# Kernel optimization log

Hardware: AMD Instinct MI355X
Metric: run time of the kernel (lower is better)

The kernel has to match this reference:

```python
import jax, jax.numpy as jnp
import numpy as np

N_HEAD = 16
WINDOW = 128
CAUSAL = False


def setup_inputs() -> dict:
    key = jax.random.key(0)
    ks = jax.random.split(key, 5)
    B, T, D = 1, 4096, 1024
    x = jax.random.normal(ks[0], (B, T, D), dtype=jnp.float32)
    w_in = jax.random.normal(ks[1], (3 * D, D), dtype=jnp.float32) * 0.02
    b_in = jax.random.normal(ks[2], (3 * D,), dtype=jnp.float32) * 0.02
    w_out = jax.random.normal(ks[3], (D, D), dtype=jnp.float32) * 0.02
    b_out = jax.random.normal(ks[4], (D,), dtype=jnp.float32) * 0.02
    return {"x": x, "w_in": w_in, "b_in": b_in, "w_out": w_out, "b_out": b_out}


def _window_attention(x, w_in, b_in, w_out, b_out):
    B, T, D = x.shape
    H = N_HEAD
    hd = D // H
    scale = 1.0 / jnp.sqrt(jnp.float32(hd))

    # fused in-projection, as in torch nn.MultiheadAttention (y = x @ W^T + b)
    qkv = jnp.einsum('btd,ed->bte', x, w_in) + b_in  # (B, T, 3D)
    q, k, v = jnp.split(qkv, 3, axis=-1)
    # (B, H, T, hd)
    q = q.reshape(B, T, H, hd).transpose(0, 2, 1, 3)
    k = k.reshape(B, T, H, hd).transpose(0, 2, 1, 3)
    v = v.reshape(B, T, H, hd).transpose(0, 2, 1, 3)

    scores = jnp.einsum('bhqd,bhkd->bhqk', q, k) * scale  # (B, H, T, T)

    idx = jnp.arange(T)
    diff = idx[:, None] - idx[None, :]
    if CAUSAL:
        allowed = (diff >= 0) & (diff <= WINDOW)
    else:
        allowed = jnp.abs(diff) <= WINDOW
    NEG = jnp.float32(-1e30)
    scores = jnp.where(allowed[None, None, :, :], scores, NEG)

    attn = jax.nn.softmax(scores, axis=-1)
    ctx = jnp.einsum('bhqk,bhkd->bhqd', attn, v)  # (B, H, T, hd)
    ctx = ctx.transpose(0, 2, 1, 3).reshape(B, T, D)
    out = jnp.einsum('btd,ed->bte', ctx, w_out) + b_out
    return x + out  # residual, as in the module


def reference(x, w_in, b_in, w_out, b_out):
    return _window_attention(x, w_in, b_in, w_out, b_out)
```

## Files before the change

kernel.cpp:

```cpp
#include <hip/hip_runtime.h>

#define T_SEQ 4096
#define DMODEL 1024
#define NHEAD 16
#define HDIM 64
#define WIN 128

typedef __attribute__((ext_vector_type(8))) short bf16x8;
typedef __attribute__((ext_vector_type(4))) float f32x4;
typedef __attribute__((ext_vector_type(4))) unsigned short u16x4;

__device__ __forceinline__ unsigned short f2bf(float f) {
  unsigned int u = __builtin_bit_cast(unsigned int, f);
  return (unsigned short)((u + 0x7fffu + ((u >> 16) & 1u)) >> 16);
}

__device__ __forceinline__ void gload_lds16(const unsigned short* g,
                                            unsigned short* l) {
  __builtin_amdgcn_global_load_lds(
      (const __attribute__((address_space(1))) void*)g,
      (__attribute__((address_space(3))) void*)l, 16, 0, 0);
}

__global__ void convert_all(const float* __restrict__ x,
                            const float* __restrict__ w_in,
                            const float* __restrict__ w_out,
                            unsigned short* __restrict__ x_bf,
                            unsigned short* __restrict__ w_in_bf,
                            unsigned short* __restrict__ w_out_bf) {
  int stride = gridDim.x * blockDim.x;
  int t0 = blockIdx.x * blockDim.x + threadIdx.x;
#define CVT(SRC, DST, N4)                                          \
  for (int i = t0; i < (N4); i += stride) {                        \
    float4 v = reinterpret_cast<const float4*>(SRC)[i];            \
    u16x4 o;                                                       \
    o.x = f2bf(v.x); o.y = f2bf(v.y); o.z = f2bf(v.z); o.w = f2bf(v.w); \
    reinterpret_cast<u16x4*>(DST)[i] = o;                          \
  }
  CVT(x, x_bf, T_SEQ * DMODEL / 4)
  CVT(w_in, w_in_bf, 3 * DMODEL * DMODEL / 4)
  CVT(w_out, w_out_bf, DMODEL * DMODEL / 4)
#undef CVT
}

template <int EPI, int BM, int BN>
__global__ __launch_bounds__(256) void gemm_db(
    const unsigned short* __restrict__ A,
    const unsigned short* __restrict__ B,
    const float* __restrict__ bias,
    unsigned short* __restrict__ q_buf,
    unsigned short* __restrict__ k_buf,
    unsigned short* __restrict__ vt_buf,
    const float* __restrict__ x_res,
    float* __restrict__ out) {
  const int K = DMODEL;
  constexpr int NT = DMODEL / 64;
  constexpr int SM = BM / 2, SN = BN / 2;
  constexpr int MR = SM / 16, NR = SN / 16;
  constexpr int AL = BM / 32, BL = BN / 32;
  __shared__ __align__(16) unsigned short As[2 * BM * 64];
  __shared__ __align__(16) unsigned short Bs[2 * BN * 64];

  int tid = threadIdx.x;
  int lane = tid & 63, wave = tid >> 6;
  int wr = wave >> 1, wc = wave & 1;
  int lo = lane & 15, hi = lane >> 4;
  int t0 = blockIdx.y * BM, e0 = blockIdx.x * BN;

  f32x4 acc[MR][NR];
#pragma unroll
  for (int m = 0; m < MR; ++m)
#pragma unroll
    for (int n = 0; n < NR; ++n) acc[m][n] = (f32x4){0.f, 0.f, 0.f, 0.f};

  int c8 = (tid & 7) ^ ((tid >> 3) & 7);
  int srow = tid >> 3;
  const unsigned short* AbaseG = A + (size_t)(t0 + srow) * K + c8 * 8;
  const unsigned short* BbaseG = B + (size_t)(e0 + srow) * K + c8 * 8;
  unsigned short* ldsAu = As + wave * 512;
  unsigned short* ldsBu = Bs + wave * 512;

  auto stage = [&](int tt) {
    int k0 = tt * 64;
    int ab = (tt & 1) * (BM * 64);
    int bb = (tt & 1) * (BN * 64);
#pragma unroll
    for (int l = 0; l < AL; ++l)
      gload_lds16(AbaseG + (size_t)l * 32 * K + k0, ldsAu + l * 2048 + ab);
#pragma unroll
    for (int l = 0; l < BL; ++l)
      gload_lds16(BbaseG + (size_t)l * 32 * K + k0, ldsBu + l * 2048 + bb);
  };

  stage(0);
  asm volatile("s_waitcnt vmcnt(0) lgkmcnt(0)\n\ts_barrier" ::: "memory");

  for (int t = 0; t < NT; ++t) {
    if (t + 1 < NT) stage(t + 1);
    const unsigned short* Ab = As + (t & 1) * (BM * 64);
    const unsigned short* Bb = Bs + (t & 1) * (BN * 64);
    bf16x8 af[MR][2], bfr[NR][2];
#pragma unroll
    for (int m = 0; m < MR; ++m) {
      int row = wr * SM + m * 16 + lo;
#pragma unroll
      for (int ks = 0; ks < 2; ++ks)
        af[m][ks] = *reinterpret_cast<const bf16x8*>(
            &Ab[row * 64 + (((ks << 2) + hi) ^ (row & 7)) * 8]);
    }
#pragma unroll
    for (int n = 0; n < NR; ++n) {
      int row = wc * SN + n * 16 + lo;
#pragma unroll
      for (int ks = 0; ks < 2; ++ks)
        bfr[n][ks] = *reinterpret_cast<const bf16x8*>(
            &Bb[row * 64 + (((ks << 2) + hi) ^ (row & 7)) * 8]);
    }
#pragma unroll
    for (int ks = 0; ks < 2; ++ks)
#pragma unroll
      for (int m = 0; m < MR; ++m)
#pragma unroll
        for (int n = 0; n < NR; ++n)
          acc[m][n] = __builtin_amdgcn_mfma_f32_16x16x32_bf16(af[m][ks], bfr[n][ks],
                                                              acc[m][n], 0, 0, 0);
    asm volatile("s_waitcnt vmcnt(0) lgkmcnt(0)\n\ts_barrier" ::: "memory");
  }

  int t0w = t0 + wr * SM;
  int e0w = e0 + wc * SN;
#pragma unroll
  for (int m = 0; m < MR; ++m) {
#pragma unroll
    for (int n = 0; n < NR; ++n) {
      int e = e0w + n * 16 + lo;
      float bv = bias[e];
      if (EPI == 0) {
        int part = e >> 10;
        int h = (e >> 6) & 15;
        int d = e & 63;
        if (part == 2) {
          int t = t0w + m * 16 + hi * 4;
          u16x4 pk;
          pk.x = f2bf(acc[m][n][0] + bv);
          pk.y = f2bf(acc[m][n][1] + bv);
          pk.z = f2bf(acc[m][n][2] + bv);
          pk.w = f2bf(acc[m][n][3] + bv);
          *reinterpret_cast<u16x4*>(&vt_buf[((size_t)(h * HDIM + d)) * T_SEQ + t]) = pk;
        } else {
          unsigned short* dst = (part == 0) ? q_buf : k_buf;
#pragma unroll
          for (int j = 0; j < 4; ++j) {
            int t = t0w + m * 16 + hi * 4 + j;
            dst[((size_t)h * T_SEQ + t) * HDIM + d] = f2bf(acc[m][n][j] + bv);
          }
        }
      } else {
#pragma unroll
        for (int j = 0; j < 4; ++j) {
          int t = t0w + m * 16 + hi * 4 + j;
          size_t idx = (size_t)t * DMODEL + e;
          out[idx] = acc[m][n][j] + bv + x_res[idx];
        }
      }
    }
  }
}

__global__ __launch_bounds__(256) void win_attn(
    const unsigned short* __restrict__ q_buf,
    const unsigned short* __restrict__ k_buf,
    const unsigned short* __restrict__ vt_buf,
    unsigned short* __restrict__ ctx) {
  __shared__ __align__(16) unsigned short p_lds[4][2][16 * 40];
  int tid = threadIdx.x;
  int wave = tid >> 6;
  int lane = tid & 63;
  int lo = lane & 15, hi = lane >> 4;

  int id = blockIdx.x;
  int sw = (id & 7) * (512 / 8) + (id >> 3);
  int job = sw * 4 + wave;
  int h = job >> 7;
  int q0 = (job & 127) * 32;
  const float SC = 0.18033688011112042f;

  bf16x8 aq[2][2];
#pragma unroll
  for (int u = 0; u < 2; ++u) {
    const unsigned short* qrow =
        q_buf + ((size_t)h * T_SEQ + q0 + u * 16 + lo) * HDIM + hi * 8;
    aq[u][0] = *reinterpret_cast<const bf16x8*>(qrow);
    aq[u][1] = *reinterpret_cast<const bf16x8*>(qrow + 32);
  }

  float L[2][4] = {{0.f, 0.f, 0.f, 0.f}, {0.f, 0.f, 0.f, 0.f}};
  f32x4 o[2][4];
#pragma unroll
  for (int u = 0; u < 2; ++u)
#pragma unroll
    for (int n = 0; n < 4; ++n) o[u][n] = (f32x4){0.f, 0.f, 0.f, 0.f};

  int jstart = q0 - WIN; if (jstart < 0) jstart = 0;
  int jend = q0 + 32 + WIN; if (jend > T_SEQ) jend = T_SEQ;

  bf16x8 kc[2][2];
#pragma unroll
  for (int c = 0; c < 2; ++c) {
    const unsigned short* kp =
        k_buf + ((size_t)h * T_SEQ + jstart + c * 16 + lo) * HDIM + hi * 8;
    kc[c][0] = *reinterpret_cast<const bf16x8*>(kp);
    kc[c][1] = *reinterpret_cast<const bf16x8*>(kp + 32);
  }

  for (int j0 = jstart; j0 < jend; j0 += 32) {
    int jn = (j0 + 32 < jend) ? j0 + 32 : jstart;
    bf16x8 kn[2][2];
#pragma unroll
    for (int c = 0; c < 2; ++c) {
      const unsigned short* kp =
          k_buf + ((size_t)h * T_SEQ + jn + c * 16 + lo) * HDIM + hi * 8;
      kn[c][0] = *reinterpret_cast<const bf16x8*>(kp);
      kn[c][1] = *reinterpret_cast<const bf16x8*>(kp + 32);
    }
    bf16x8 bv[4];
#pragma unroll
    for (int n = 0; n < 4; ++n)
      bv[n] = *reinterpret_cast<const bf16x8*>(
          vt_buf + ((size_t)(h * HDIM + n * 16 + lo)) * T_SEQ + j0 + hi * 8);
#pragma unroll
    for (int u = 0; u < 2; ++u) {
#pragma unroll
      for (int c = 0; c < 2; ++c) {
        f32x4 z = (f32x4){0.f, 0.f, 0.f, 0.f};
        z = __builtin_amdgcn_mfma_f32_16x16x32_bf16(aq[u][0], kc[c][0], z, 0, 0, 0);
        z = __builtin_amdgcn_mfma_f32_16x16x32_bf16(aq[u][1], kc[c][1], z, 0, 0, 0);
        int kj = j0 + c * 16 + lo;
#pragma unroll
        for (int j = 0; j < 4; ++j) {
          int q = q0 + u * 16 + hi * 4 + j;
          bool ok = (q - kj <= WIN) && (kj - q <= WIN);
          float p = ok ? __builtin_amdgcn_exp2f(z[j] * SC) : 0.f;
          L[u][j] += p;
          p_lds[wave][u][(hi * 4 + j) * 40 + c * 16 + lo] = f2bf(p);
        }
      }
    }
    bf16x8 pa[2];
    pa[0] = *reinterpret_cast<const bf16x8*>(&p_lds[wave][0][lo * 40 + hi * 8]);
    pa[1] = *reinterpret_cast<const bf16x8*>(&p_lds[wave][1][lo * 40 + hi * 8]);
#pragma unroll
    for (int n = 0; n < 4; ++n) {
      o[0][n] = __builtin_amdgcn_mfma_f32_16x16x32_bf16(pa[0], bv[n], o[0][n], 0, 0, 0);
      o[1][n] = __builtin_amdgcn_mfma_f32_16x16x32_bf16(pa[1], bv[n], o[1][n], 0, 0, 0);
    }
#pragma unroll
    for (int c = 0; c < 2; ++c) {
      kc[c][0] = kn[c][0];
      kc[c][1] = kn[c][1];
    }
  }
#pragma unroll
  for (int u = 0; u < 2; ++u)
#pragma unroll
    for (int j = 0; j < 4; ++j) {
#pragma unroll
      for (int w = 1; w < 16; w <<= 1) L[u][j] += __shfl_xor(L[u][j], w, 64);
    }
#pragma unroll
  for (int u = 0; u < 2; ++u)
#pragma unroll
    for (int j = 0; j < 4; ++j) {
      int t = q0 + u * 16 + hi * 4 + j;
      float inv = 1.f / L[u][j];
#pragma unroll
      for (int n = 0; n < 4; ++n)
        ctx[(size_t)t * DMODEL + h * HDIM + n * 16 + lo] = f2bf(o[u][n][j] * inv);
    }
}

extern "C" void kernel_launch(void* const* d_in, const int* in_sizes, int n_in,
                              void* d_out, int out_size, void* d_ws, size_t ws_size,
                              hipStream_t stream) {
  const float* x = (const float*)d_in[0];
  const float* w_in = (const float*)d_in[1];
  const float* b_in = (const float*)d_in[2];
  const float* w_out = (const float*)d_in[3];
  const float* b_out = (const float*)d_in[4];
  float* out = (float*)d_out;

  char* ws = (char*)d_ws;
  size_t off = 0;
  auto take = [&](size_t bytes) {
    char* p = ws + off;
    off += (bytes + 255) & ~(size_t)255;
    return p;
  };
  unsigned short* x_bf = (unsigned short*)take((size_t)T_SEQ * DMODEL * 2);
  unsigned short* w_in_bf = (unsigned short*)take((size_t)3 * DMODEL * DMODEL * 2);
  unsigned short* w_out_bf = (unsigned short*)take((size_t)DMODEL * DMODEL * 2);
  unsigned short* q_buf = (unsigned short*)take((size_t)T_SEQ * DMODEL * 2);
  unsigned short* k_buf = (unsigned short*)take((size_t)T_SEQ * DMODEL * 2);
  unsigned short* vt_buf = (unsigned short*)take((size_t)T_SEQ * DMODEL * 2 + 8192);
  unsigned short* ctx = (unsigned short*)take((size_t)T_SEQ * DMODEL * 2);

  convert_all<<<2048, 256, 0, stream>>>(x, w_in, w_out, x_bf, w_in_bf, w_out_bf);

  dim3 g1(3 * DMODEL / 192, T_SEQ / 128);
  gemm_db<0, 128, 192><<<g1, 256, 0, stream>>>(x_bf, w_in_bf, b_in, q_buf, k_buf,
                                               vt_buf, nullptr, nullptr);

  win_attn<<<512, 256, 0, stream>>>(q_buf, k_buf, vt_buf, ctx);

  dim3 g2(DMODEL / 64, T_SEQ / 128);
  gemm_db<1, 128, 64><<<g2, 256, 0, stream>>>(ctx, w_out_bf, b_out, nullptr, nullptr,
                                              nullptr, x, out);
}
```

Measured before the change: 89.20 us.

## Enlarge GEMM tiles to 256 rows with 512 threads and XCD-aware block mapping

Both projection GEMMs now use 256-row tiles computed by 8 waves (512 threads), and the 2D grid becomes a 1D grid of 256 blocks. Block indices are remapped so blocks landing on the same XCD share row strips, which should improve L2 reuse of the A operand. The inner loop now loads fragments per k-substep to lower register pressure. The trade-off is fewer blocks, exactly 256 for 256 CUs, so there is no spare occupancy, plus more LDS per block. The out-projection's remap covers 16 column tiles of 64, which matches D=1024.

```diff
diff --git a/kernel.cpp b/kernel.cpp
--- a/kernel.cpp
+++ b/kernel.cpp
@@ -44,7 +44,7 @@
 }
 
 template <int EPI, int BM, int BN>
-__global__ __launch_bounds__(256) void gemm_db(
+__global__ __launch_bounds__(512) void gemm_db(
     const unsigned short* __restrict__ A,
     const unsigned short* __restrict__ B,
     const float* __restrict__ bias,
@@ -55,9 +55,9 @@
     float* __restrict__ out) {
   const int K = DMODEL;
   constexpr int NT = DMODEL / 64;
-  constexpr int SM = BM / 2, SN = BN / 2;
+  constexpr int SM = 64, SN = BN / 2;
   constexpr int MR = SM / 16, NR = SN / 16;
-  constexpr int AL = BM / 32, BL = BN / 32;
+  constexpr int AL = BM / 64, BL = BN / 64;
   __shared__ __align__(16) unsigned short As[2 * BM * 64];
   __shared__ __align__(16) unsigned short Bs[2 * BN * 64];
 
@@ -65,7 +65,12 @@
   int lane = tid & 63, wave = tid >> 6;
   int wr = wave >> 1, wc = wave & 1;
   int lo = lane & 15, hi = lane >> 4;
-  int t0 = blockIdx.y * BM, e0 = blockIdx.x * BN;
+
+  int idx = blockIdx.x;
+  int xcd = idx & 7, j = idx >> 3;
+  int bx = j & 15;
+  int by = xcd * 2 + (j >> 4);
+  int t0 = by * BM, e0 = bx * BN;
 
   f32x4 acc[MR][NR];
 #pragma unroll
@@ -86,10 +91,10 @@
     int bb = (tt & 1) * (BN * 64);
 #pragma unroll
     for (int l = 0; l < AL; ++l)
-      gload_lds16(AbaseG + (size_t)l * 32 * K + k0, ldsAu + l * 2048 + ab);
+      gload_lds16(AbaseG + (size_t)l * 64 * K + k0, ldsAu + l * 4096 + ab);
 #pragma unroll
     for (int l = 0; l < BL; ++l)
-      gload_lds16(BbaseG + (size_t)l * 32 * K + k0, ldsBu + l * 2048 + bb);
+      gload_lds16(BbaseG + (size_t)l * 64 * K + k0, ldsBu + l * 4096 + bb);
   };
 
   stage(0);
@@ -99,31 +104,28 @@
     if (t + 1 < NT) stage(t + 1);
     const unsigned short* Ab = As + (t & 1) * (BM * 64);
     const unsigned short* Bb = Bs + (t & 1) * (BN * 64);
-    bf16x8 af[MR][2], bfr[NR][2];
-#pragma unroll
-    for (int m = 0; m < MR; ++m) {
-      int row = wr * SM + m * 16 + lo;
-#pragma unroll
-      for (int ks = 0; ks < 2; ++ks)
-        af[m][ks] = *reinterpret_cast<const bf16x8*>(
+#pragma unroll
+    for (int ks = 0; ks < 2; ++ks) {
+      bf16x8 af[MR], bfr[NR];
+#pragma unroll
+      for (int m = 0; m < MR; ++m) {
+        int row = wr * SM + m * 16 + lo;
+        af[m] = *reinterpret_cast<const bf16x8*>(
             &Ab[row * 64 + (((ks << 2) + hi) ^ (row & 7)) * 8]);
-    }
-#pragma unroll
-    for (int n = 0; n < NR; ++n) {
-      int row = wc * SN + n * 16 + lo;
-#pragma unroll
-      for (int ks = 0; ks < 2; ++ks)
-        bfr[n][ks] = *reinterpret_cast<const bf16x8*>(
+      }
+#pragma unroll
+      for (int n = 0; n < NR; ++n) {
+        int row = wc * SN + n * 16 + lo;
+        bfr[n] = *reinterpret_cast<const bf16x8*>(
             &Bb[row * 64 + (((ks << 2) + hi) ^ (row & 7)) * 8]);
-    }
-#pragma unroll
-    for (int ks = 0; ks < 2; ++ks)
+      }
 #pragma unroll
       for (int m = 0; m < MR; ++m)
 #pragma unroll
         for (int n = 0; n < NR; ++n)
-          acc[m][n] = __builtin_amdgcn_mfma_f32_16x16x32_bf16(af[m][ks], bfr[n][ks],
+          acc[m][n] = __builtin_amdgcn_mfma_f32_16x16x32_bf16(af[m], bfr[n],
                                                               acc[m][n], 0, 0, 0);
+    }
     asm volatile("s_waitcnt vmcnt(0) lgkmcnt(0)\n\ts_barrier" ::: "memory");
   }
 
@@ -150,17 +152,17 @@
         } else {
           unsigned short* dst = (part == 0) ? q_buf : k_buf;
 #pragma unroll
-          for (int j = 0; j < 4; ++j) {
-            int t = t0w + m * 16 + hi * 4 + j;
-            dst[((size_t)h * T_SEQ + t) * HDIM + d] = f2bf(acc[m][n][j] + bv);
+          for (int jj = 0; jj < 4; ++jj) {
+            int t = t0w + m * 16 + hi * 4 + jj;
+            dst[((size_t)h * T_SEQ + t) * HDIM + d] = f2bf(acc[m][n][jj] + bv);
           }
         }
       } else {
 #pragma unroll
-        for (int j = 0; j < 4; ++j) {
-          int t = t0w + m * 16 + hi * 4 + j;
-          size_t idx = (size_t)t * DMODEL + e;
-          out[idx] = acc[m][n][j] + bv + x_res[idx];
+        for (int jj = 0; jj < 4; ++jj) {
+          int t = t0w + m * 16 + hi * 4 + jj;
+          size_t idxo = (size_t)t * DMODEL + e;
+          out[idxo] = acc[m][n][jj] + bv + x_res[idxo];
         }
       }
     }
@@ -237,12 +239,12 @@
         z = __builtin_amdgcn_mfma_f32_16x16x32_bf16(aq[u][1], kc[c][1], z, 0, 0, 0);
         int kj = j0 + c * 16 + lo;
 #pragma unroll
-        for (int j = 0; j < 4; ++j) {
-          int q = q0 + u * 16 + hi * 4 + j;
+        for (int jq = 0; jq < 4; ++jq) {
+          int q = q0 + u * 16 + hi * 4 + jq;
           bool ok = (q - kj <= WIN) && (kj - q <= WIN);
-          float p = ok ? __builtin_amdgcn_exp2f(z[j] * SC) : 0.f;
-          L[u][j] += p;
-          p_lds[wave][u][(hi * 4 + j) * 40 + c * 16 + lo] = f2bf(p);
+          float p = ok ? __builtin_amdgcn_exp2f(z[jq] * SC) : 0.f;
+          L[u][jq] += p;
+          p_lds[wave][u][(hi * 4 + jq) * 40 + c * 16 + lo] = f2bf(p);
         }
       }
     }
@@ -263,19 +265,19 @@
 #pragma unroll
   for (int u = 0; u < 2; ++u)
 #pragma unroll
-    for (int j = 0; j < 4; ++j) {
-#pragma unroll
-      for (int w = 1; w < 16; w <<= 1) L[u][j] += __shfl_xor(L[u][j], w, 64);
+    for (int jq = 0; jq < 4; ++jq) {
+#pragma unroll
+      for (int w = 1; w < 16; w <<= 1) L[u][jq] += __shfl_xor(L[u][jq], w, 64);
     }
 #pragma unroll
   for (int u = 0; u < 2; ++u)
 #pragma unroll
-    for (int j = 0; j < 4; ++j) {
-      int t = q0 + u * 16 + hi * 4 + j;
-      float inv = 1.f / L[u][j];
+    for (int jq = 0; jq < 4; ++jq) {
+      int t = q0 + u * 16 + hi * 4 + jq;
+      float inv = 1.f / L[u][jq];
 #pragma unroll
       for (int n = 0; n < 4; ++n)
-        ctx[(size_t)t * DMODEL + h * HDIM + n * 16 + lo] = f2bf(o[u][n][j] * inv);
+        ctx[(size_t)t * DMODEL + h * HDIM + n * 16 + lo] = f2bf(o[u][n][jq] * inv);
     }
 }
 
@@ -306,13 +308,11 @@
 
   convert_all<<<2048, 256, 0, stream>>>(x, w_in, w_out, x_bf, w_in_bf, w_out_bf);
 
-  dim3 g1(3 * DMODEL / 192, T_SEQ / 128);
-  gemm_db<0, 128, 192><<<g1, 256, 0, stream>>>(x_bf, w_in_bf, b_in, q_buf, k_buf,
-                                               vt_buf, nullptr, nullptr);
+  gemm_db<0, 256, 192><<<256, 512, 0, stream>>>(x_bf, w_in_bf, b_in, q_buf, k_buf,
+                                                vt_buf, nullptr, nullptr);
 
   win_attn<<<512, 256, 0, stream>>>(q_buf, k_buf, vt_buf, ctx);
 
-  dim3 g2(DMODEL / 64, T_SEQ / 128);
-  gemm_db<1, 128, 64><<<g2, 256, 0, stream>>>(ctx, w_out_bf, b_out, nullptr, nullptr,
-                                              nullptr, x, out);
-}
+  gemm_db<1, 256, 64><<<256, 512, 0, stream>>>(ctx, w_out_bf, b_out, nullptr, nullptr,
+                                               nullptr, x, out);
+}
```

After: 89.48 us. No clear change (+0.3%).

## Split attention key range across wave pairs and merge partial results via LDS

Applied to the files above, without the earlier changes.

Each query tile in the windowed attention kernel is now processed by two waves, each handling half of the key range, and the grid doubles to 1024 blocks. Partial outputs and row sums are exchanged through a new shared-memory buffer and combined, with each wave writing half of the rows. The change also raises wave priority around MFMA instructions and wraps the GEMM template in two named kernels. It aims to add parallelism and shorten the serial key loop per wave, at the cost of extra LDS traffic, a block barrier and larger shared memory use.

```diff
diff --git a/kernel.cpp b/kernel.cpp
--- a/kernel.cpp
+++ b/kernel.cpp
@@ -44,7 +44,7 @@
 }
 
 template <int EPI, int BM, int BN>
-__global__ __launch_bounds__(256) void gemm_db(
+__device__ __forceinline__ void gemm_body(
     const unsigned short* __restrict__ A,
     const unsigned short* __restrict__ B,
     const float* __restrict__ bias,
@@ -150,21 +150,35 @@
         } else {
           unsigned short* dst = (part == 0) ? q_buf : k_buf;
 #pragma unroll
-          for (int j = 0; j < 4; ++j) {
-            int t = t0w + m * 16 + hi * 4 + j;
-            dst[((size_t)h * T_SEQ + t) * HDIM + d] = f2bf(acc[m][n][j] + bv);
+          for (int jj = 0; jj < 4; ++jj) {
+            int t = t0w + m * 16 + hi * 4 + jj;
+            dst[((size_t)h * T_SEQ + t) * HDIM + d] = f2bf(acc[m][n][jj] + bv);
           }
         }
       } else {
 #pragma unroll
-        for (int j = 0; j < 4; ++j) {
-          int t = t0w + m * 16 + hi * 4 + j;
-          size_t idx = (size_t)t * DMODEL + e;
-          out[idx] = acc[m][n][j] + bv + x_res[idx];
+        for (int jj = 0; jj < 4; ++jj) {
+          int t = t0w + m * 16 + hi * 4 + jj;
+          size_t idxo = (size_t)t * DMODEL + e;
+          out[idxo] = acc[m][n][jj] + bv + x_res[idxo];
         }
       }
     }
   }
+}
+
+__global__ __launch_bounds__(256) void qkv_gemm(
+    const unsigned short* __restrict__ A, const unsigned short* __restrict__ B,
+    const float* __restrict__ bias, unsigned short* __restrict__ q_buf,
+    unsigned short* __restrict__ k_buf, unsigned short* __restrict__ vt_buf) {
+  gemm_body<0, 128, 192>(A, B, bias, q_buf, k_buf, vt_buf, nullptr, nullptr);
+}
+
+__global__ __launch_bounds__(256) void out_gemm(
+    const unsigned short* __restrict__ A, const unsigned short* __restrict__ B,
+    const float* __restrict__ bias, const float* __restrict__ x_res,
+    float* __restrict__ out) {
+  gemm_body<1, 128, 64>(A, B, bias, nullptr, nullptr, nullptr, x_res, out);
 }
 
 __global__ __launch_bounds__(256) void win_attn(
@@ -173,14 +187,16 @@
     const unsigned short* __restrict__ vt_buf,
     unsigned short* __restrict__ ctx) {
   __shared__ __align__(16) unsigned short p_lds[4][2][16 * 40];
+  __shared__ float mrg[4][64][21];
   int tid = threadIdx.x;
   int wave = tid >> 6;
   int lane = tid & 63;
   int lo = lane & 15, hi = lane >> 4;
 
   int id = blockIdx.x;
-  int sw = (id & 7) * (512 / 8) + (id >> 3);
-  int job = sw * 4 + wave;
+  int sw = (id & 7) * (1024 / 8) + (id >> 3);
+  int job = sw * 2 + (wave >> 1);
+  int kh = wave & 1;
   int h = job >> 7;
   int q0 = (job & 127) * 32;
   const float SC = 0.18033688011112042f;
@@ -203,18 +219,22 @@
 
   int jstart = q0 - WIN; if (jstart < 0) jstart = 0;
   int jend = q0 + 32 + WIN; if (jend > T_SEQ) jend = T_SEQ;
+  int nt = (jend - jstart + 31) >> 5;
+  int half = (nt + 1) >> 1;
+  int my_start = jstart + (kh ? half : 0) * 32;
+  int my_end = kh ? jend : (jstart + half * 32);
 
   bf16x8 kc[2][2];
 #pragma unroll
   for (int c = 0; c < 2; ++c) {
     const unsigned short* kp =
-        k_buf + ((size_t)h * T_SEQ + jstart + c * 16 + lo) * HDIM + hi * 8;
+        k_buf + ((size_t)h * T_SEQ + my_start + c * 16 + lo) * HDIM + hi * 8;
     kc[c][0] = *reinterpret_cast<const bf16x8*>(kp);
     kc[c][1] = *reinterpret_cast<const bf16x8*>(kp + 32);
   }
 
-  for (int j0 = jstart; j0 < jend; j0 += 32) {
-    int jn = (j0 + 32 < jend) ? j0 + 32 : jstart;
+  for (int j0 = my_start; j0 < my_end; j0 += 32) {
+    int jn = (j0 + 32 < my_end) ? j0 + 32 : my_start;
     bf16x8 kn[2][2];
 #pragma unroll
     for (int c = 0; c < 2; ++c) {
@@ -233,50 +253,95 @@
 #pragma unroll
       for (int c = 0; c < 2; ++c) {
         f32x4 z = (f32x4){0.f, 0.f, 0.f, 0.f};
+        __builtin_amdgcn_s_setprio(1);
         z = __builtin_amdgcn_mfma_f32_16x16x32_bf16(aq[u][0], kc[c][0], z, 0, 0, 0);
         z = __builtin_amdgcn_mfma_f32_16x16x32_bf16(aq[u][1], kc[c][1], z, 0, 0, 0);
+        __builtin_amdgcn_s_setprio(0);
         int kj = j0 + c * 16 + lo;
 #pragma unroll
-        for (int j = 0; j < 4; ++j) {
-          int q = q0 + u * 16 + hi * 4 + j;
+        for (int jq = 0; jq < 4; ++jq) {
+          int q = q0 + u * 16 + hi * 4 + jq;
           bool ok = (q - kj <= WIN) && (kj - q <= WIN);
-          float p = ok ? __builtin_amdgcn_exp2f(z[j] * SC) : 0.f;
-          L[u][j] += p;
-          p_lds[wave][u][(hi * 4 + j) * 40 + c * 16 + lo] = f2bf(p);
+          float p = ok ? __builtin_amdgcn_exp2f(z[jq] * SC) : 0.f;
+          L[u][jq] += p;
+          p_lds[wave][u][(hi * 4 + jq) * 40 + c * 16 + lo] = f2bf(p);
         }
       }
     }
     bf16x8 pa[2];
     pa[0] = *reinterpret_cast<const bf16x8*>(&p_lds[wave][0][lo * 40 + hi * 8]);
     pa[1] = *reinterpret_cast<const bf16x8*>(&p_lds[wave][1][lo * 40 + hi * 8]);
+    __builtin_amdgcn_s_setprio(1);
 #pragma unroll
     for (int n = 0; n < 4; ++n) {
       o[0][n] = __builtin_amdgcn_mfma_f32_16x16x32_bf16(pa[0], bv[n], o[0][n], 0, 0, 0);
       o[1][n] = __builtin_amdgcn_mfma_f32_16x16x32_bf16(pa[1], bv[n], o[1][n], 0, 0, 0);
     }
+    __builtin_amdgcn_s_setprio(0);
 #pragma unroll
     for (int c = 0; c < 2; ++c) {
       kc[c][0] = kn[c][0];
       kc[c][1] = kn[c][1];
     }
   }
-#pragma unroll
-  for (int u = 0; u < 2; ++u)
-#pragma unroll
-    for (int j = 0; j < 4; ++j) {
-#pragma unroll
-      for (int w = 1; w < 16; w <<= 1) L[u][j] += __shfl_xor(L[u][j], w, 64);
-    }
-#pragma unroll
-  for (int u = 0; u < 2; ++u)
-#pragma unroll
-    for (int j = 0; j < 4; ++j) {
-      int t = q0 + u * 16 + hi * 4 + j;
-      float inv = 1.f / L[u][j];
+
+  float* mw = &mrg[wave][lane][0];
+  if (kh == 0) {
+#pragma unroll
+    for (int n = 0; n < 4; ++n)
+#pragma unroll
+      for (int jq = 0; jq < 4; ++jq) mw[n * 4 + jq] = o[1][n][jq];
+#pragma unroll
+    for (int jq = 0; jq < 4; ++jq) mw[16 + jq] = L[1][jq];
+  } else {
+#pragma unroll
+    for (int n = 0; n < 4; ++n)
+#pragma unroll
+      for (int jq = 0; jq < 4; ++jq) mw[n * 4 + jq] = o[0][n][jq];
+#pragma unroll
+    for (int jq = 0; jq < 4; ++jq) mw[16 + jq] = L[0][jq];
+  }
+  __syncthreads();
+  const float* mr = &mrg[wave ^ 1][lane][0];
+  if (kh == 0) {
+#pragma unroll
+    for (int n = 0; n < 4; ++n)
+#pragma unroll
+      for (int jq = 0; jq < 4; ++jq) o[0][n][jq] += mr[n * 4 + jq];
+#pragma unroll
+    for (int jq = 0; jq < 4; ++jq) {
+      L[0][jq] += mr[16 + jq];
+#pragma unroll
+      for (int w = 1; w < 16; w <<= 1) L[0][jq] += __shfl_xor(L[0][jq], w, 64);
+    }
+#pragma unroll
+    for (int jq = 0; jq < 4; ++jq) {
+      int t = q0 + hi * 4 + jq;
+      float inv = 1.f / L[0][jq];
 #pragma unroll
       for (int n = 0; n < 4; ++n)
-        ctx[(size_t)t * DMODEL + h * HDIM + n * 16 + lo] = f2bf(o[u][n][j] * inv);
-    }
+        ctx[(size_t)t * DMODEL + h * HDIM + n * 16 + lo] = f2bf(o[0][n][jq] * inv);
+    }
+  } else {
+#pragma unroll
+    for (int n = 0; n < 4; ++n)
+#pragma unroll
+      for (int jq = 0; jq < 4; ++jq) o[1][n][jq] += mr[n * 4 + jq];
+#pragma unroll
+    for (int jq = 0; jq < 4; ++jq) {
+      L[1][jq] += mr[16 + jq];
+#pragma unroll
+      for (int w = 1; w < 16; w <<= 1) L[1][jq] += __shfl_xor(L[1][jq], w, 64);
+    }
+#pragma unroll
+    for (int jq = 0; jq < 4; ++jq) {
+      int t = q0 + 16 + hi * 4 + jq;
+      float inv = 1.f / L[1][jq];
+#pragma unroll
+      for (int n = 0; n < 4; ++n)
+        ctx[(size_t)t * DMODEL + h * HDIM + n * 16 + lo] = f2bf(o[1][n][jq] * inv);
+    }
+  }
 }
 
 extern "C" void kernel_launch(void* const* d_in, const int* in_sizes, int n_in,
@@ -307,12 +372,10 @@
   convert_all<<<2048, 256, 0, stream>>>(x, w_in, w_out, x_bf, w_in_bf, w_out_bf);
 
   dim3 g1(3 * DMODEL / 192, T_SEQ / 128);
-  gemm_db<0, 128, 192><<<g1, 256, 0, stream>>>(x_bf, w_in_bf, b_in, q_buf, k_buf,
-                                               vt_buf, nullptr, nullptr);
-
-  win_attn<<<512, 256, 0, stream>>>(q_buf, k_buf, vt_buf, ctx);
+  qkv_gemm<<<g1, 256, 0, stream>>>(x_bf, w_in_bf, b_in, q_buf, k_buf, vt_buf);
+
+  win_attn<<<1024, 256, 0, stream>>>(q_buf, k_buf, vt_buf, ctx);
 
   dim3 g2(DMODEL / 64, T_SEQ / 128);
-  gemm_db<1, 128, 64><<<g2, 256, 0, stream>>>(ctx, w_out_bf, b_out, nullptr, nullptr,
-                                              nullptr, x, out);
-}
+  out_gemm<<<g2, 256, 0, stream>>>(ctx, w_out_bf, b_out, x, out);
+}
```

Result: slower. 93.99 us (+5.4%).
